# Optimization experiments

Measured on AMD Instinct MI355X. Metric: run time of the kernel, lower is better.

## Reference

```python
import jax, jax.numpy as jnp
import numpy as np

EPS = 1e-4
RES_BAL = 0.3
ATTN_BAL = 0.3
CLIP = 256.0
HEADS = 4
CPH = 64  # channels per head


def _normalize(x, dims):
    # torch normalize: norm = eps + norm * sqrt(norm.numel()/x.numel())
    n = jnp.sqrt(jnp.sum(jnp.square(x), axis=dims, keepdims=True))
    alpha = 1.0 / np.sqrt(float(np.prod([x.shape[d] for d in dims])))
    return x / (EPS + alpha * n)


def _mp_weight(w, gain):
    dims = tuple(range(1, w.ndim))
    fan_in = float(np.prod(w.shape[1:]))
    return _normalize(w, dims) * (gain / np.sqrt(fan_in))


def _conv2d(x, w):
    pad = w.shape[-1] // 2
    return jax.lax.conv_general_dilated(
        x, w, (1, 1), [(pad, pad), (pad, pad)],
        dimension_numbers=('NCHW', 'OIHW', 'NCHW'))


def _mp_silu(x):
    return jax.nn.silu(x) / 0.596


def _mp_sum(a, b, t):
    return ((1.0 - t) * a + t * b) / np.sqrt((1.0 - t) ** 2 + t ** 2)


def setup_inputs() -> dict:
    key = jax.random.key(0)
    ks = jax.random.split(key, 9)
    N, Cin, Cout, Cemb, H, W = 16, 192, 256, 768, 32, 32
    return {
        'x': jax.random.normal(ks[0], (N, Cin, H, W), jnp.float32),
        'emb': jax.random.normal(ks[1], (N, Cemb), jnp.float32),
        'w_skip': jax.random.normal(ks[2], (Cout, Cin, 1, 1), jnp.float32),
        'w_res0': jax.random.normal(ks[3], (Cout, Cout, 3, 3), jnp.float32),
        'w_res1': jax.random.normal(ks[4], (Cout, Cout, 3, 3), jnp.float32),
        'w_emb': jax.random.normal(ks[5], (Cout, Cemb), jnp.float32),
        'emb_gain': jnp.float32(0.5),
        'w_qkv': jax.random.normal(ks[6], (Cout * 3, Cout, 1, 1), jnp.float32),
        'w_proj': jax.random.normal(ks[7], (Cout, Cout, 1, 1), jnp.float32),
    }


def reference(x, emb, w_skip, w_res0, w_res1, w_emb, emb_gain, w_qkv, w_proj):
    N, _, H, W = x.shape
    S = H * W
    # enc flavor: skip conv then pixel-norm over channels
    x = _conv2d(x, _mp_weight(w_skip, 1.0))
    x = _normalize(x, (1,))
    # residual branch
    y = _conv2d(_mp_silu(x), _mp_weight(w_res0, 1.0))
    c = emb @ _mp_weight(w_emb, emb_gain).T + 1.0  # [N, Cout]
    y = y * c[:, :, None, None]
    y = _conv2d(_mp_silu(y), _mp_weight(w_res1, 1.0))
    x = _mp_sum(x, y, RES_BAL)
    # cosine-normalized attention
    qkv = _conv2d(x, _mp_weight(w_qkv, 1.0))              # [N, 3*Cout, H, W]
    qkv = qkv.reshape(N, HEADS, CPH, 3, S)
    qkv = _normalize(qkv, (2,))
    q, k, v = qkv[..., 0, :], qkv[..., 1, :], qkv[..., 2, :]  # [N,h,c,S]
    att = jax.nn.softmax(
        jnp.einsum('nhcq,nhck->nhqk', q, k) / np.sqrt(CPH), axis=3)
    y = jnp.einsum('nhqk,nhck->nhcq', att, v).reshape(x.shape)
    y = _conv2d(y, _mp_weight(w_proj, 1.0))
    x = _mp_sum(x, y, ATTN_BAL)
    return jnp.clip(x, -CLIP, CLIP)
```

## Files before the change

kernel.cpp:

```cpp
#include <hip/hip_runtime.h>
#include <math.h>

#define SDIM 1024
#define COUT 256

#define EPSV     1e-4f
#define SILU_INV 1.6778523489932886f
#define MPA      0.9191450300180579f
#define MPB      0.3939192985791677f
#define LOG2E    1.4426950408889634f

typedef short s16x8 __attribute__((ext_vector_type(8)));
typedef float f32x4 __attribute__((ext_vector_type(4)));
typedef unsigned short ushort_t;

#if __has_builtin(__builtin_amdgcn_exp2f)
#define EXP2F __builtin_amdgcn_exp2f
#else
#define EXP2F exp2f
#endif

__device__ inline ushort_t f2bs(float f) {
    unsigned u = __float_as_uint(f);
    u += 0x7fffu + ((u >> 16) & 1u);
    return (ushort_t)(u >> 16);
}
__device__ inline float silu_mp(float v) { return v * SILU_INV / (1.f + __expf(-v)); }

union F8 { s16x8 v; uint4 q; };
__device__ inline s16x8 ld16(const ushort_t* p) {
    F8 r; r.q = *(const uint4*)p; return r.v;
}

typedef const __attribute__((address_space(1))) unsigned int* gas_ptr;
typedef __attribute__((address_space(3))) unsigned int* las_ptr;
__device__ inline void gld16(const void* g, void* l) {
    __builtin_amdgcn_global_load_lds((gas_ptr)g, (las_ptr)l, 16, 0, 0);
}

__global__ void zfill(uint4* z) { z[threadIdx.x] = make_uint4(0u, 0u, 0u, 0u); }

__global__ __launch_bounds__(256) void wnorm(const float* __restrict__ w,
                                             float* __restrict__ wn,
                                             int fanin,
                                             const float* __restrict__ gain_ptr)
{
    int o = blockIdx.x;
    const float* row = w + (size_t)o * fanin;
    float ss = 0.f;
    for (int i = threadIdx.x; i < fanin; i += 256) { float v = row[i]; ss += v * v; }
    for (int off = 32; off >= 1; off >>= 1) ss += __shfl_down(ss, off);
    __shared__ float red[4];
    int lane = threadIdx.x & 63, wv = threadIdx.x >> 6;
    if (lane == 0) red[wv] = ss;
    __syncthreads();
    float tot = red[0] + red[1] + red[2] + red[3];
    float gain = gain_ptr ? *gain_ptr : 1.0f;
    float scale = gain / (EPSV * sqrtf((float)fanin) + sqrtf(tot));
    for (int i = threadIdx.x; i < fanin; i += 256)
        wn[(size_t)o * fanin + i] = row[i] * scale;
}

template<bool REORDER, bool QPERM>
__global__ __launch_bounds__(256) void wnorm_bf16(const float* __restrict__ w,
                                                  ushort_t* __restrict__ wn,
                                                  int fanin)
{
    int o = blockIdx.x;
    const float* row = w + (size_t)o * fanin;
    float ss = 0.f;
    for (int i = threadIdx.x; i < fanin; i += 256) { float v = row[i]; ss += v * v; }
    for (int off = 32; off >= 1; off >>= 1) ss += __shfl_down(ss, off);
    __shared__ float red[4];
    int lane = threadIdx.x & 63, wv = threadIdx.x >> 6;
    if (lane == 0) red[wv] = ss;
    __syncthreads();
    float tot = red[0] + red[1] + red[2] + red[3];
    float scale = 1.0f / (EPSV * sqrtf((float)fanin) + sqrtf(tot));
    int orow = o;
    if (QPERM) { int h = o / 192, rem = o % 192; orow = (rem % 3) * 256 + h * 64 + rem / 3; }
    for (int i = threadIdx.x; i < fanin; i += 256) {
        int kd = i;
        if (REORDER) { int ci = i / 9; int r9 = i - ci * 9; kd = r9 * 256 + ci; }
        wn[(size_t)orow * fanin + kd] = f2bs(row[i] * scale);
    }
}

__global__ __launch_bounds__(256) void emb_mm(const float* __restrict__ emb,
                                              const float* __restrict__ wemb,
                                              float* __restrict__ cvec)
{
    int n = blockIdx.x;
    int co = threadIdx.x;
    const float* e  = emb  + (size_t)n * 768;
    const float* wr = wemb + (size_t)co * 768;
    float s = 0.f;
    for (int i = 0; i < 768; i++) s = fmaf(e[i], wr[i], s);
    cvec[n * COUT + co] = s + 1.0f;
}

__global__ __launch_bounds__(256) void prep_xT(const float* __restrict__ x,
                                               ushort_t* __restrict__ xT)
{
    const int n = blockIdx.z, ci0 = blockIdx.y * 64, s0 = blockIdx.x * 64;
    const int tid = threadIdx.x;
    __shared__ float T[64 * 65];
#pragma unroll
    for (int i = 0; i < 16; i++) {
        int ch = tid + i * 256; int row = ch >> 6, cc = ch & 63;
        T[row * 65 + cc] = x[((size_t)n * 192 + ci0 + row) * SDIM + s0 + cc];
    }
    __syncthreads();
#pragma unroll
    for (int i = 0; i < 2; i++) {
        int ch = tid + i * 256; int srow = ch >> 3, c8 = ch & 7;
        ushort_t tmp[8];
#pragma unroll
        for (int j = 0; j < 8; j++) tmp[j] = f2bs(T[(c8 * 8 + j) * 65 + srow]);
        *(uint4*)(xT + ((size_t)n * SDIM + s0 + srow) * 192 + ci0 + c8 * 8) = *(uint4*)tmp;
    }
}

__global__ __launch_bounds__(256, 2) void skip_fused(const ushort_t* __restrict__ Wp,
                                                     const ushort_t* __restrict__ xT,
                                                     float* __restrict__ xn,
                                                     ushort_t* __restrict__ sxT)
{
    const int n = blockIdx.z, s0 = blockIdx.x * 32;
    const int tid = threadIdx.x, w = tid >> 6, lane = tid & 63;
    const int tx = lane & 15, quad = lane >> 4;

    __shared__ ushort_t As[256 * 72];
    __shared__ ushort_t Bs[32 * 72];
    __shared__ float csum[4][32];

    f32x4 acc[4][2];
#pragma unroll
    for (int a = 0; a < 4; a++)
#pragma unroll
        for (int b = 0; b < 2; b++) acc[a][b] = (f32x4){0.f, 0.f, 0.f, 0.f};

    for (int k0 = 0; k0 < 192; k0 += 64) {
        __syncthreads();
#pragma unroll
        for (int i = 0; i < 8; i++) {
            int ch = tid + i * 256; int row = ch >> 3, c8 = ch & 7;
            *(uint4*)&As[row * 72 + c8 * 8] = *(const uint4*)(Wp + (size_t)row * 192 + k0 + c8 * 8);
        }
        {
            int row = tid >> 3, c8 = tid & 7;
            *(uint4*)&Bs[row * 72 + c8 * 8] =
                *(const uint4*)(xT + ((size_t)n * SDIM + s0 + row) * 192 + k0 + c8 * 8);
        }
        __syncthreads();
#pragma unroll
        for (int kc = 0; kc < 2; kc++) {
            s16x8 af[4], bf_[2];
#pragma unroll
            for (int mt = 0; mt < 4; mt++) af[mt] = ld16(&As[(w * 64 + mt * 16 + tx) * 72 + kc * 32 + quad * 8]);
#pragma unroll
            for (int nt = 0; nt < 2; nt++) bf_[nt] = ld16(&Bs[(nt * 16 + tx) * 72 + kc * 32 + quad * 8]);
#pragma unroll
            for (int mt = 0; mt < 4; mt++)
#pragma unroll
                for (int nt = 0; nt < 2; nt++)
                    acc[mt][nt] = __builtin_amdgcn_mfma_f32_16x16x32_bf16(af[mt], bf_[nt], acc[mt][nt], 0, 0, 0);
        }
    }

#pragma unroll
    for (int nt = 0; nt < 2; nt++) {
        float s2 = 0.f;
#pragma unroll
        for (int mt = 0; mt < 4; mt++)
#pragma unroll
            for (int r = 0; r < 4; r++) s2 = fmaf(acc[mt][nt][r], acc[mt][nt][r], s2);
        s2 += __shfl_xor(s2, 16); s2 += __shfl_xor(s2, 32);
        if (quad == 0) csum[w][nt * 16 + tx] = s2;
    }
    __syncthreads();
    float f[2];
#pragma unroll
    for (int nt = 0; nt < 2; nt++) {
        int col = nt * 16 + tx;
        float tot = csum[0][col] + csum[1][col] + csum[2][col] + csum[3][col];
        f[nt] = 1.f / (EPSV + sqrtf(tot) * 0.0625f);
    }
    ushort_t* Ls = As;
    float* xb = xn + (size_t)n * COUT * SDIM;
#pragma unroll
    for (int mt = 0; mt < 4; mt++)
#pragma unroll
        for (int r = 0; r < 4; r++) {
            int co = w * 64 + mt * 16 + quad * 4 + r;
#pragma unroll
            for (int nt = 0; nt < 2; nt++) {
                int sp = s0 + nt * 16 + tx;
                float v = acc[mt][nt][r] * f[nt];
                xb[(size_t)co * SDIM + sp] = v;
                Ls[(nt * 16 + tx) * 264 + co] = f2bs(silu_mp(v));
            }
        }
    __syncthreads();
#pragma unroll
    for (int i = 0; i < 4; i++) {
        int ch = tid + i * 256; int row = ch >> 5, c32 = ch & 31;
        *(uint4*)(sxT + ((size_t)n * SDIM + s0 + row) * 256 + c32 * 8) = *(uint4*)&Ls[row * 264 + c32 * 8];
    }
}

template<int KDIM, bool GATHER3, int MODE>
__global__ __launch_bounds__(256, 2) void gemm_glds(const ushort_t* __restrict__ Wp,
                                                    const ushort_t* __restrict__ Bsrc,
                                                    const ushort_t* __restrict__ zbuf,
                                                    float* RX, float* Outf,
                                                    ushort_t* OutT, ushort_t* Vout,
                                                    const float* __restrict__ cvec)
{
    const int n = blockIdx.z, co0 = blockIdx.y * 128, s0 = blockIdx.x * 64;
    const int tid = threadIdx.x, w = tid >> 6, lane = tid & 63;
    const int tx = lane & 15, quad = lane >> 4;
    const int wm = w >> 1, ws = w & 1;
    const int l8 = lane & 7, ld = lane >> 3;
    const int swz = (l8 ^ ld) * 8;

    __shared__ ushort_t SH[2 * 12288];

    const ushort_t* bn = Bsrc + (size_t)n * SDIM * 256;

    auto stageA = [&](int p, int k0) {
        ushort_t* Ab = SH + p * 12288;
#pragma unroll
        for (int j = 0; j < 4; j++) {
            int row0 = w * 32 + j * 8;
            gld16(Wp + (size_t)(co0 + row0 + ld) * KDIM + k0 + swz, Ab + row0 * 64);
        }
    };
    auto stageB = [&](int p, int k0) {
        ushort_t* Bb = SH + p * 12288 + 8192;
        int ci0 = k0, dy = 0, dx = 0;
        if (GATHER3) { int seg = k0 >> 8; ci0 = k0 & 255; int s3 = seg / 3; dy = s3 - 1; dx = seg - s3 * 3 - 1; }
#pragma unroll
        for (int j = 0; j < 2; j++) {
            int row0 = w * 16 + j * 8;
            const ushort_t* g;
            if (GATHER3) {
                int pix = s0 + row0 + ld;
                int h = (pix >> 5) + dy, wx = (pix & 31) + dx;
                bool valid = ((unsigned)h < 32u) && ((unsigned)wx < 32u);
                g = valid ? (bn + (size_t)((h << 5) + wx) * 256 + ci0 + swz) : zbuf;
            } else {
                g = bn + (size_t)(s0 + row0 + ld) * 256 + k0 + swz;
            }
            gld16(g, Bb + row0 * 64);
        }
    };

    f32x4 acc[4][2];
#pragma unroll
    for (int a = 0; a < 4; a++)
#pragma unroll
        for (int b = 0; b < 2; b++) acc[a][b] = (f32x4){0.f, 0.f, 0.f, 0.f};

    constexpr int NK = KDIM / 64;
    stageA(0, 0); stageB(0, 0);
    __syncthreads();

    for (int kt = 0; kt < NK; kt++) {
        int p = kt & 1;
        if (kt + 1 < NK) { stageA(p ^ 1, (kt + 1) * 64); stageB(p ^ 1, (kt + 1) * 64); }
        const ushort_t* Ab = SH + p * 12288;
        const ushort_t* Bb = Ab + 8192;
#pragma unroll
        for (int kc = 0; kc < 2; kc++) {
            int koff = ((kc * 4 + quad) ^ (tx & 7)) * 8;
            s16x8 af[4], bfv[2];
#pragma unroll
            for (int mt = 0; mt < 4; mt++) af[mt]  = ld16(&Ab[(wm * 64 + mt * 16 + tx) * 64 + koff]);
#pragma unroll
            for (int nt = 0; nt < 2; nt++) bfv[nt] = ld16(&Bb[(ws * 32 + nt * 16 + tx) * 64 + koff]);
#pragma unroll
            for (int mt = 0; mt < 4; mt++)
#pragma unroll
                for (int nt = 0; nt < 2; nt++)
                    acc[mt][nt] = __builtin_amdgcn_mfma_f32_16x16x32_bf16(af[mt], bfv[nt], acc[mt][nt], 0, 0, 0);
        }
        __syncthreads();
    }

    if (MODE == 4) {
        float scl[2];
#pragma unroll
        for (int nt = 0; nt < 2; nt++) {
            float s2 = 0.f;
#pragma unroll
            for (int mt = 0; mt < 4; mt++)
#pragma unroll
                for (int r = 0; r < 4; r++) s2 = fmaf(acc[mt][nt][r], acc[mt][nt][r], s2);
            s2 += __shfl_xor(s2, 16); s2 += __shfl_xor(s2, 32);
            float fac = (co0 < 256) ? (0.125f * LOG2E) : 1.0f;
            scl[nt] = fac / (EPSV + sqrtf(s2) * 0.125f);
        }
#pragma unroll
        for (int mt = 0; mt < 4; mt++)
#pragma unroll
            for (int nt = 0; nt < 2; nt++)
#pragma unroll
                for (int r = 0; r < 4; r++) acc[mt][nt][r] *= scl[nt];

        if (co0 < 512) {
            ushort_t* Ls = SH;
#pragma unroll
            for (int mt = 0; mt < 4; mt++)
#pragma unroll
                for (int nt = 0; nt < 2; nt++)
#pragma unroll
                    for (int r = 0; r < 4; r++)
                        Ls[(ws * 32 + nt * 16 + tx) * 136 + wm * 64 + mt * 16 + quad * 4 + r] = f2bs(acc[mt][nt][r]);
            __syncthreads();
#pragma unroll
            for (int i = 0; i < 4; i++) {
                int ch = tid + i * 256; int row = ch >> 4, c16 = ch & 15;
                *(uint4*)(OutT + ((size_t)n * SDIM + s0 + row) * 512 + co0 + c16 * 8) = *(uint4*)&Ls[row * 136 + c16 * 8];
            }
        } else {
            ushort_t* Ls = SH;
#pragma unroll
            for (int mt = 0; mt < 4; mt++)
#pragma unroll
                for (int nt = 0; nt < 2; nt++)
#pragma unroll
                    for (int r = 0; r < 4; r++)
                        Ls[(wm * 64 + mt * 16 + quad * 4 + r) * 72 + ws * 32 + nt * 16 + tx] = f2bs(acc[mt][nt][r]);
            __syncthreads();
#pragma unroll
            for (int i = 0; i < 4; i++) {
                int ch = tid + i * 256; int row = ch >> 3, c8 = ch & 7;
                *(uint4*)(Vout + ((size_t)n * 256 + (co0 - 512) + row) * SDIM + s0 + c8 * 8) = *(uint4*)&Ls[row * 72 + c8 * 8];
            }
        }
    }
    if (MODE == 1) {
        float cm[4][4];
#pragma unroll
        for (int mt = 0; mt < 4; mt++)
#pragma unroll
            for (int r = 0; r < 4; r++)
                cm[mt][r] = cvec[n * COUT + co0 + wm * 64 + mt * 16 + quad * 4 + r];
        ushort_t* Ls = SH;
#pragma unroll
        for (int mt = 0; mt < 4; mt++)
#pragma unroll
            for (int nt = 0; nt < 2; nt++)
#pragma unroll
                for (int r = 0; r < 4; r++) {
                    float v = silu_mp(acc[mt][nt][r] * cm[mt][r]);
                    Ls[(ws * 32 + nt * 16 + tx) * 136 + wm * 64 + mt * 16 + quad * 4 + r] = f2bs(v);
                }
        __syncthreads();
#pragma unroll
        for (int i = 0; i < 4; i++) {
            int ch = tid + i * 256; int row = ch >> 4, c16 = ch & 15;
            *(uint4*)(OutT + ((size_t)n * SDIM + s0 + row) * 256 + co0 + c16 * 8) = *(uint4*)&Ls[row * 136 + c16 * 8];
        }
    }
    if (MODE == 2) {
        ushort_t* Ls = SH;
#pragma unroll
        for (int mt = 0; mt < 4; mt++)
#pragma unroll
            for (int r = 0; r < 4; r++) {
                int col = wm * 64 + mt * 16 + quad * 4 + r;
                float* xp = RX + ((size_t)n * COUT + co0 + col) * SDIM + s0 + ws * 32;
#pragma unroll
                for (int nt = 0; nt < 2; nt++) {
                    float v = MPA * xp[nt * 16 + tx] + MPB * acc[mt][nt][r];
                    xp[nt * 16 + tx] = v;
                    Ls[(ws * 32 + nt * 16 + tx) * 136 + col] = f2bs(v);
                }
            }
        __syncthreads();
#pragma unroll
        for (int i = 0; i < 4; i++) {
            int ch = tid + i * 256; int row = ch >> 4, c16 = ch & 15;
            *(uint4*)(OutT + ((size_t)n * SDIM + s0 + row) * 256 + co0 + c16 * 8) = *(uint4*)&Ls[row * 136 + c16 * 8];
        }
    }
    if (MODE == 3) {
#pragma unroll
        for (int mt = 0; mt < 4; mt++)
#pragma unroll
            for (int r = 0; r < 4; r++) {
                int co = co0 + wm * 64 + mt * 16 + quad * 4 + r;
                const float* xp = RX + ((size_t)n * COUT + co) * SDIM + s0 + ws * 32;
                float* op = Outf + ((size_t)n * COUT + co) * SDIM + s0 + ws * 32;
#pragma unroll
                for (int nt = 0; nt < 2; nt++) {
                    float v = MPA * xp[nt * 16 + tx] + MPB * acc[mt][nt][r];
                    op[nt * 16 + tx] = fminf(fmaxf(v, -256.f), 256.f);
                }
            }
    }
}

__global__ __launch_bounds__(256, 2) void attn_mfma(const ushort_t* __restrict__ qkT,
                                                    const ushort_t* __restrict__ vbuf,
                                                    ushort_t* __restrict__ aT)
{
    const int n = blockIdx.z, head = blockIdx.y, q0 = blockIdx.x * 128;
    const int tid = threadIdx.x, w = tid >> 6, lane = tid & 63;
    const int tx = lane & 15, quad = lane >> 4;

    __shared__ ushort_t Pl[4][32 * 72];

    const size_t nb = (size_t)n * SDIM;
    const int qw = q0 + w * 32;

    s16x8 qf[2][2];
#pragma unroll
    for (int mt = 0; mt < 2; mt++)
#pragma unroll
        for (int kc = 0; kc < 2; kc++)
            qf[mt][kc] = ld16(qkT + (nb + qw + mt * 16 + tx) * 512 + head * 64 + kc * 32 + quad * 8);

    f32x4 acco[2][4];
    float lpart[2][4];
#pragma unroll
    for (int mt = 0; mt < 2; mt++)
#pragma unroll
        for (int nt = 0; nt < 4; nt++) acco[mt][nt] = (f32x4){0.f, 0.f, 0.f, 0.f};
#pragma unroll
    for (int mt = 0; mt < 2; mt++)
#pragma unroll
        for (int r = 0; r < 4; r++) lpart[mt][r] = 0.f;

    const ushort_t* kbase = qkT + nb * 512 + 256 + head * 64;
    const ushort_t* vbase = vbuf + ((size_t)n * 256 + head * 64) * SDIM;

    for (int kt = 0; kt < 16; kt++) {
        int k0 = kt * 64;
        s16x8 kf[4][2];
#pragma unroll
        for (int nt = 0; nt < 4; nt++)
#pragma unroll
            for (int kc = 0; kc < 2; kc++)
                kf[nt][kc] = ld16(kbase + (size_t)(k0 + nt * 16 + tx) * 512 + kc * 32 + quad * 8);

        f32x4 accs[2][4];
#pragma unroll
        for (int mt = 0; mt < 2; mt++)
#pragma unroll
            for (int nt = 0; nt < 4; nt++) accs[mt][nt] = (f32x4){0.f, 0.f, 0.f, 0.f};
#pragma unroll
        for (int kc = 0; kc < 2; kc++)
#pragma unroll
            for (int nt = 0; nt < 4; nt++)
#pragma unroll
                for (int mt = 0; mt < 2; mt++)
                    accs[mt][nt] = __builtin_amdgcn_mfma_f32_16x16x32_bf16(
                        qf[mt][kc], kf[nt][kc], accs[mt][nt], 0, 0, 0);

#pragma unroll
        for (int mt = 0; mt < 2; mt++)
#pragma unroll
            for (int nt = 0; nt < 4; nt++)
#pragma unroll
                for (int r = 0; r < 4; r++) {
                    float p = EXP2F(accs[mt][nt][r]);
                    lpart[mt][r] += p;
                    Pl[w][(mt * 16 + quad * 4 + r) * 72 + nt * 16 + tx] = f2bs(p);
                }
        asm volatile("s_waitcnt lgkmcnt(0)" ::: "memory");

        s16x8 vf[4][2], pf[2][2];
#pragma unroll
        for (int nt = 0; nt < 4; nt++)
#pragma unroll
            for (int kc = 0; kc < 2; kc++)
                vf[nt][kc] = ld16(vbase + (size_t)(nt * 16 + tx) * SDIM + k0 + kc * 32 + quad * 8);
#pragma unroll
        for (int mt = 0; mt < 2; mt++)
#pragma unroll
            for (int kc = 0; kc < 2; kc++)
                pf[mt][kc] = ld16(&Pl[w][(mt * 16 + tx) * 72 + kc * 32 + quad * 8]);
#pragma unroll
        for (int kc = 0; kc < 2; kc++)
#pragma unroll
            for (int nt = 0; nt < 4; nt++)
#pragma unroll
                for (int mt = 0; mt < 2; mt++)
                    acco[mt][nt] = __builtin_amdgcn_mfma_f32_16x16x32_bf16(
                        pf[mt][kc], vf[nt][kc], acco[mt][nt], 0, 0, 0);
    }

    float inv[2][4];
#pragma unroll
    for (int mt = 0; mt < 2; mt++)
#pragma unroll
        for (int r = 0; r < 4; r++) {
            float l = lpart[mt][r];
            l += __shfl_xor(l, 1); l += __shfl_xor(l, 2);
            l += __shfl_xor(l, 4); l += __shfl_xor(l, 8);
            inv[mt][r] = 1.0f / l;
        }

#pragma unroll
    for (int mt = 0; mt < 2; mt++)
#pragma unroll
        for (int nt = 0; nt < 4; nt++)
#pragma unroll
            for (int r = 0; r < 4; r++)
                Pl[w][(mt * 16 + quad * 4 + r) * 72 + nt * 16 + tx] = f2bs(acco[mt][nt][r] * inv[mt][r]);
    asm volatile("s_waitcnt lgkmcnt(0)" ::: "memory");
    ushort_t* dst = aT + (nb + qw) * 256 + head * 64;
#pragma unroll
    for (int i = 0; i < 4; i++) {
        int ch = lane + i * 64; int row = ch >> 3, c8 = ch & 7;
        *(uint4*)(dst + (size_t)row * 256 + c8 * 8) = *(uint4*)&Pl[w][row * 72 + c8 * 8];
    }
}

extern "C" void kernel_launch(void* const* d_in, const int* in_sizes, int n_in,
                              void* d_out, int out_size, void* d_ws, size_t ws_size,
                              hipStream_t stream)
{
    const float* x      = (const float*)d_in[0];
    const float* emb    = (const float*)d_in[1];
    const float* w_skip = (const float*)d_in[2];
    const float* w_res0 = (const float*)d_in[3];
    const float* w_res1 = (const float*)d_in[4];
    const float* w_emb  = (const float*)d_in[5];
    const float* e_gain = (const float*)d_in[6];
    const float* w_qkv  = (const float*)d_in[7];
    const float* w_proj = (const float*)d_in[8];
    float* out = (float*)d_out;

    char* p = (char*)d_ws;
    auto alloc = [&](size_t bytes) { void* r = (void*)p; p += (bytes + 255) & ~(size_t)255; return r; };
    ushort_t* wskip_bf = (ushort_t*)alloc(256 * 192 * 2);
    ushort_t* wres0_bf = (ushort_t*)alloc(256 * 2304 * 2);
    ushort_t* wres1_bf = (ushort_t*)alloc(256 * 2304 * 2);
    ushort_t* wqkv_bf  = (ushort_t*)alloc(768 * 256 * 2);
    ushort_t* wproj_bf = (ushort_t*)alloc(256 * 256 * 2);
    float*    wemb_n   = (float*)alloc(256 * 768 * 4);
    float*    cvec     = (float*)alloc(16 * 256 * 4);
    ushort_t* zbuf     = (ushort_t*)alloc(1024);
    ushort_t* xT   = (ushort_t*)alloc((size_t)16 * 1024 * 192 * 2);
    ushort_t* sxT  = (ushort_t*)alloc((size_t)16 * 1024 * 256 * 2);
    ushort_t* ysT  = (ushort_t*)alloc((size_t)16 * 1024 * 256 * 2);
    ushort_t* x2T  = (ushort_t*)alloc((size_t)16 * 1024 * 256 * 2);
    ushort_t* aT   = (ushort_t*)alloc((size_t)16 * 1024 * 256 * 2);
    float*    xn   = (float*)alloc((size_t)16 * 256 * 1024 * 4);
    ushort_t* qkT  = (ushort_t*)alloc((size_t)16 * 1024 * 512 * 2);
    ushort_t* vbuf = (ushort_t*)alloc((size_t)16 * 256 * 1024 * 2);

    zfill<<<1, 64, 0, stream>>>((uint4*)zbuf);
    wnorm_bf16<false, false><<<256, 256, 0, stream>>>(w_skip, wskip_bf, 192);
    wnorm_bf16<true,  false><<<256, 256, 0, stream>>>(w_res0, wres0_bf, 2304);
    wnorm_bf16<true,  false><<<256, 256, 0, stream>>>(w_res1, wres1_bf, 2304);
    wnorm_bf16<false, true ><<<768, 256, 0, stream>>>(w_qkv,  wqkv_bf,  256);
    wnorm_bf16<false, false><<<256, 256, 0, stream>>>(w_proj, wproj_bf, 256);
    wnorm<<<256, 256, 0, stream>>>(w_emb, wemb_n, 768, e_gain);

    emb_mm<<<16, 256, 0, stream>>>(emb, wemb_n, cvec);
    prep_xT<<<dim3(16, 3, 16), 256, 0, stream>>>(x, xT);

    skip_fused<<<dim3(32, 1, 16), 256, 0, stream>>>(wskip_bf, xT, xn, sxT);
    gemm_glds<2304, true, 1><<<dim3(16, 2, 16), 256, 0, stream>>>(wres0_bf, sxT, zbuf, nullptr, nullptr, ysT, nullptr, cvec);
    gemm_glds<2304, true, 2><<<dim3(16, 2, 16), 256, 0, stream>>>(wres1_bf, ysT, zbuf, xn, nullptr, x2T, nullptr, nullptr);
    gemm_glds<256, false, 4><<<dim3(16, 6, 16), 256, 0, stream>>>(wqkv_bf, x2T, zbuf, nullptr, nullptr, qkT, vbuf, nullptr);
    attn_mfma<<<dim3(8, 4, 16), 256, 0, stream>>>(qkT, vbuf, aT);
    gemm_glds<256, false, 3><<<dim3(16, 2, 16), 256, 0, stream>>>(wproj_bf, aT, zbuf, xn, out, nullptr, nullptr, nullptr);
}
```

Baseline: 301.2 us.

## Stage K/V in swizzled LDS for attention and merge prep kernels

The attention kernel now gives each wave 64 query rows instead of 32, so each block covers 256 queries. K and V tiles are double-buffered in LDS through global_load_lds with an XOR swizzle, and the four waves share them instead of each wave loading K/V from global memory on its own. The P scratch buffer uses the same swizzle to avoid bank conflicts. Separately, all weight-normalisation kernels, the x transpose and the zero fill are merged into one launch, and the emb weight normalisation is folded into emb_mm. The attention grid halves to 256 blocks at occupancy 1 with more registers per thread, which may leave some CUs idle.

```diff
diff --git a/kernel.cpp b/kernel.cpp
--- a/kernel.cpp
+++ b/kernel.cpp
@@ -38,87 +38,82 @@
     __builtin_amdgcn_global_load_lds((gas_ptr)g, (las_ptr)l, 16, 0, 0);
 }
 
-__global__ void zfill(uint4* z) { z[threadIdx.x] = make_uint4(0u, 0u, 0u, 0u); }
-
-__global__ __launch_bounds__(256) void wnorm(const float* __restrict__ w,
-                                             float* __restrict__ wn,
-                                             int fanin,
-                                             const float* __restrict__ gain_ptr)
+__global__ __launch_bounds__(256) void prep_all(
+    const float* __restrict__ w_skip, const float* __restrict__ w_res0,
+    const float* __restrict__ w_res1, const float* __restrict__ w_qkv,
+    const float* __restrict__ w_proj, const float* __restrict__ x,
+    ushort_t* wskip_bf, ushort_t* wres0_bf, ushort_t* wres1_bf,
+    ushort_t* wqkv_bf, ushort_t* wproj_bf, ushort_t* xT, uint4* zbuf)
 {
-    int o = blockIdx.x;
-    const float* row = w + (size_t)o * fanin;
+    __shared__ float T[64 * 65];
+    const int b = blockIdx.x, tid = threadIdx.x;
+
+    if (b >= 2560) {
+        if (tid < 64) zbuf[tid] = make_uint4(0u, 0u, 0u, 0u);
+        return;
+    }
+    if (b >= 1792) {
+        int b2 = b - 1792;
+        int n = b2 / 48, rem = b2 % 48;
+        int ci0 = (rem / 16) * 64, s0 = (rem & 15) * 64;
+#pragma unroll
+        for (int i = 0; i < 16; i++) {
+            int ch = tid + i * 256; int row = ch >> 6, cc = ch & 63;
+            T[row * 65 + cc] = x[((size_t)n * 192 + ci0 + row) * SDIM + s0 + cc];
+        }
+        __syncthreads();
+#pragma unroll
+        for (int i = 0; i < 2; i++) {
+            int ch = tid + i * 256; int srow = ch >> 3, c8 = ch & 7;
+            ushort_t tmp[8];
+#pragma unroll
+            for (int j = 0; j < 8; j++) tmp[j] = f2bs(T[(c8 * 8 + j) * 65 + srow]);
+            *(uint4*)(xT + ((size_t)n * SDIM + s0 + srow) * 192 + ci0 + c8 * 8) = *(uint4*)tmp;
+        }
+        return;
+    }
+    const float* src; ushort_t* dst; int fanin, mode, o;
+    if      (b < 256)  { src = w_skip; dst = wskip_bf; fanin = 192;  mode = 0; o = b; }
+    else if (b < 512)  { src = w_res0; dst = wres0_bf; fanin = 2304; mode = 1; o = b - 256; }
+    else if (b < 768)  { src = w_res1; dst = wres1_bf; fanin = 2304; mode = 1; o = b - 512; }
+    else if (b < 1536) { src = w_qkv;  dst = wqkv_bf;  fanin = 256;  mode = 2; o = b - 768; }
+    else               { src = w_proj; dst = wproj_bf; fanin = 256;  mode = 0; o = b - 1536; }
+
+    const float* row = src + (size_t)o * fanin;
     float ss = 0.f;
-    for (int i = threadIdx.x; i < fanin; i += 256) { float v = row[i]; ss += v * v; }
+    for (int i = tid; i < fanin; i += 256) { float v = row[i]; ss += v * v; }
     for (int off = 32; off >= 1; off >>= 1) ss += __shfl_down(ss, off);
-    __shared__ float red[4];
-    int lane = threadIdx.x & 63, wv = threadIdx.x >> 6;
-    if (lane == 0) red[wv] = ss;
+    int lane = tid & 63, wv = tid >> 6;
+    if (lane == 0) T[wv] = ss;
     __syncthreads();
-    float tot = red[0] + red[1] + red[2] + red[3];
-    float gain = gain_ptr ? *gain_ptr : 1.0f;
-    float scale = gain / (EPSV * sqrtf((float)fanin) + sqrtf(tot));
-    for (int i = threadIdx.x; i < fanin; i += 256)
-        wn[(size_t)o * fanin + i] = row[i] * scale;
-}
-
-template<bool REORDER, bool QPERM>
-__global__ __launch_bounds__(256) void wnorm_bf16(const float* __restrict__ w,
-                                                  ushort_t* __restrict__ wn,
-                                                  int fanin)
-{
-    int o = blockIdx.x;
-    const float* row = w + (size_t)o * fanin;
-    float ss = 0.f;
-    for (int i = threadIdx.x; i < fanin; i += 256) { float v = row[i]; ss += v * v; }
-    for (int off = 32; off >= 1; off >>= 1) ss += __shfl_down(ss, off);
-    __shared__ float red[4];
-    int lane = threadIdx.x & 63, wv = threadIdx.x >> 6;
-    if (lane == 0) red[wv] = ss;
-    __syncthreads();
-    float tot = red[0] + red[1] + red[2] + red[3];
+    float tot = T[0] + T[1] + T[2] + T[3];
     float scale = 1.0f / (EPSV * sqrtf((float)fanin) + sqrtf(tot));
     int orow = o;
-    if (QPERM) { int h = o / 192, rem = o % 192; orow = (rem % 3) * 256 + h * 64 + rem / 3; }
-    for (int i = threadIdx.x; i < fanin; i += 256) {
+    if (mode == 2) { int h = o / 192, rem = o % 192; orow = (rem % 3) * 256 + h * 64 + rem / 3; }
+    for (int i = tid; i < fanin; i += 256) {
         int kd = i;
-        if (REORDER) { int ci = i / 9; int r9 = i - ci * 9; kd = r9 * 256 + ci; }
-        wn[(size_t)orow * fanin + kd] = f2bs(row[i] * scale);
+        if (mode == 1) { int ci = i / 9; int r9 = i - ci * 9; kd = r9 * 256 + ci; }
+        dst[(size_t)orow * fanin + kd] = f2bs(row[i] * scale);
     }
 }
 
 __global__ __launch_bounds__(256) void emb_mm(const float* __restrict__ emb,
-                                              const float* __restrict__ wemb,
+                                              const float* __restrict__ w_emb,
+                                              const float* __restrict__ gain_ptr,
                                               float* __restrict__ cvec)
 {
     int n = blockIdx.x;
     int co = threadIdx.x;
-    const float* e  = emb  + (size_t)n * 768;
-    const float* wr = wemb + (size_t)co * 768;
-    float s = 0.f;
-    for (int i = 0; i < 768; i++) s = fmaf(e[i], wr[i], s);
-    cvec[n * COUT + co] = s + 1.0f;
-}
-
-__global__ __launch_bounds__(256) void prep_xT(const float* __restrict__ x,
-                                               ushort_t* __restrict__ xT)
-{
-    const int n = blockIdx.z, ci0 = blockIdx.y * 64, s0 = blockIdx.x * 64;
-    const int tid = threadIdx.x;
-    __shared__ float T[64 * 65];
-#pragma unroll
-    for (int i = 0; i < 16; i++) {
-        int ch = tid + i * 256; int row = ch >> 6, cc = ch & 63;
-        T[row * 65 + cc] = x[((size_t)n * 192 + ci0 + row) * SDIM + s0 + cc];
-    }
-    __syncthreads();
-#pragma unroll
-    for (int i = 0; i < 2; i++) {
-        int ch = tid + i * 256; int srow = ch >> 3, c8 = ch & 7;
-        ushort_t tmp[8];
-#pragma unroll
-        for (int j = 0; j < 8; j++) tmp[j] = f2bs(T[(c8 * 8 + j) * 65 + srow]);
-        *(uint4*)(xT + ((size_t)n * SDIM + s0 + srow) * 192 + ci0 + c8 * 8) = *(uint4*)tmp;
-    }
+    const float* e  = emb   + (size_t)n * 768;
+    const float* wr = w_emb + (size_t)co * 768;
+    float ss = 0.f, dot = 0.f;
+    for (int i = 0; i < 768; i++) {
+        float wv = wr[i];
+        ss  = fmaf(wv, wv, ss);
+        dot = fmaf(e[i], wv, dot);
+    }
+    float scale = gain_ptr[0] / (EPSV * sqrtf(768.0f) + sqrtf(ss));
+    cvec[n * COUT + co] = dot * scale + 1.0f;
 }
 
 __global__ __launch_bounds__(256, 2) void skip_fused(const ushort_t* __restrict__ Wp,
@@ -403,99 +398,115 @@
     }
 }
 
-__global__ __launch_bounds__(256, 2) void attn_mfma(const ushort_t* __restrict__ qkT,
+__global__ __launch_bounds__(256, 1) void attn_mfma(const ushort_t* __restrict__ qkT,
                                                     const ushort_t* __restrict__ vbuf,
                                                     ushort_t* __restrict__ aT)
 {
-    const int n = blockIdx.z, head = blockIdx.y, q0 = blockIdx.x * 128;
+    const int n = blockIdx.z, head = blockIdx.y, q0 = blockIdx.x * 256;
     const int tid = threadIdx.x, w = tid >> 6, lane = tid & 63;
     const int tx = lane & 15, quad = lane >> 4;
-
-    __shared__ ushort_t Pl[4][32 * 72];
+    const int l8 = lane & 7, ld = lane >> 3;
+    const int swz = (l8 ^ ld) * 8;
+
+    __shared__ ushort_t Kst[2][4096];
+    __shared__ ushort_t Vst[2][4096];
+    __shared__ ushort_t Pl[4][4096];
 
     const size_t nb = (size_t)n * SDIM;
-    const int qw = q0 + w * 32;
-
-    s16x8 qf[2][2];
-#pragma unroll
-    for (int mt = 0; mt < 2; mt++)
+    const int qw = q0 + w * 64;
+    const ushort_t* kg = qkT + nb * 512 + 256 + head * 64;
+    const ushort_t* vg = vbuf + ((size_t)n * 256 + head * 64) * SDIM;
+
+    auto stage = [&](int p, int k0) {
+#pragma unroll
+        for (int j = 0; j < 2; j++) {
+            int row0 = w * 16 + j * 8;
+            gld16(kg + (size_t)(k0 + row0 + ld) * 512 + swz, &Kst[p][row0 * 64]);
+            gld16(vg + (size_t)(row0 + ld) * SDIM + k0 + swz, &Vst[p][row0 * 64]);
+        }
+    };
+
+    s16x8 qf[4][2];
+#pragma unroll
+    for (int mt = 0; mt < 4; mt++)
 #pragma unroll
         for (int kc = 0; kc < 2; kc++)
             qf[mt][kc] = ld16(qkT + (nb + qw + mt * 16 + tx) * 512 + head * 64 + kc * 32 + quad * 8);
 
-    f32x4 acco[2][4];
-    float lpart[2][4];
-#pragma unroll
-    for (int mt = 0; mt < 2; mt++)
+    f32x4 acco[4][4];
+    float lpart[4][4];
+#pragma unroll
+    for (int mt = 0; mt < 4; mt++)
 #pragma unroll
         for (int nt = 0; nt < 4; nt++) acco[mt][nt] = (f32x4){0.f, 0.f, 0.f, 0.f};
 #pragma unroll
-    for (int mt = 0; mt < 2; mt++)
+    for (int mt = 0; mt < 4; mt++)
 #pragma unroll
         for (int r = 0; r < 4; r++) lpart[mt][r] = 0.f;
 
-    const ushort_t* kbase = qkT + nb * 512 + 256 + head * 64;
-    const ushort_t* vbase = vbuf + ((size_t)n * 256 + head * 64) * SDIM;
+    stage(0, 0);
+    __syncthreads();
 
     for (int kt = 0; kt < 16; kt++) {
-        int k0 = kt * 64;
-        s16x8 kf[4][2];
-#pragma unroll
-        for (int nt = 0; nt < 4; nt++)
-#pragma unroll
-            for (int kc = 0; kc < 2; kc++)
-                kf[nt][kc] = ld16(kbase + (size_t)(k0 + nt * 16 + tx) * 512 + kc * 32 + quad * 8);
-
-        f32x4 accs[2][4];
-#pragma unroll
-        for (int mt = 0; mt < 2; mt++)
+        int p = kt & 1;
+        if (kt < 15) stage(p ^ 1, (kt + 1) * 64);
+
+        f32x4 accs[4][4];
+#pragma unroll
+        for (int mt = 0; mt < 4; mt++)
 #pragma unroll
             for (int nt = 0; nt < 4; nt++) accs[mt][nt] = (f32x4){0.f, 0.f, 0.f, 0.f};
 #pragma unroll
-        for (int kc = 0; kc < 2; kc++)
-#pragma unroll
-            for (int nt = 0; nt < 4; nt++)
-#pragma unroll
-                for (int mt = 0; mt < 2; mt++)
+        for (int kc = 0; kc < 2; kc++) {
+            int koff = ((kc * 4 + quad) ^ (tx & 7)) * 8;
+#pragma unroll
+            for (int nt = 0; nt < 4; nt++) {
+                s16x8 kf = ld16(&Kst[p][(nt * 16 + tx) * 64 + koff]);
+#pragma unroll
+                for (int mt = 0; mt < 4; mt++)
                     accs[mt][nt] = __builtin_amdgcn_mfma_f32_16x16x32_bf16(
-                        qf[mt][kc], kf[nt][kc], accs[mt][nt], 0, 0, 0);
-
-#pragma unroll
-        for (int mt = 0; mt < 2; mt++)
-#pragma unroll
-            for (int nt = 0; nt < 4; nt++)
-#pragma unroll
-                for (int r = 0; r < 4; r++) {
-                    float p = EXP2F(accs[mt][nt][r]);
-                    lpart[mt][r] += p;
-                    Pl[w][(mt * 16 + quad * 4 + r) * 72 + nt * 16 + tx] = f2bs(p);
+                        qf[mt][kc], kf, accs[mt][nt], 0, 0, 0);
+            }
+        }
+
+#pragma unroll
+        for (int mt = 0; mt < 4; mt++)
+#pragma unroll
+            for (int r = 0; r < 4; r++) {
+                int row = mt * 16 + quad * 4 + r;
+                int rx = row & 7;
+#pragma unroll
+                for (int nt = 0; nt < 4; nt++) {
+                    float pv = EXP2F(accs[mt][nt][r]);
+                    lpart[mt][r] += pv;
+                    int slot = (nt * 2 + (tx >> 3)) ^ rx;
+                    Pl[w][row * 64 + slot * 8 + (tx & 7)] = f2bs(pv);
                 }
+            }
         asm volatile("s_waitcnt lgkmcnt(0)" ::: "memory");
 
-        s16x8 vf[4][2], pf[2][2];
-#pragma unroll
-        for (int nt = 0; nt < 4; nt++)
-#pragma unroll
-            for (int kc = 0; kc < 2; kc++)
-                vf[nt][kc] = ld16(vbase + (size_t)(nt * 16 + tx) * SDIM + k0 + kc * 32 + quad * 8);
-#pragma unroll
-        for (int mt = 0; mt < 2; mt++)
-#pragma unroll
-            for (int kc = 0; kc < 2; kc++)
-                pf[mt][kc] = ld16(&Pl[w][(mt * 16 + tx) * 72 + kc * 32 + quad * 8]);
-#pragma unroll
-        for (int kc = 0; kc < 2; kc++)
-#pragma unroll
-            for (int nt = 0; nt < 4; nt++)
-#pragma unroll
-                for (int mt = 0; mt < 2; mt++)
+#pragma unroll
+        for (int kc = 0; kc < 2; kc++) {
+            int koff = ((kc * 4 + quad) ^ (tx & 7)) * 8;
+            s16x8 pf[4];
+#pragma unroll
+            for (int mt = 0; mt < 4; mt++)
+                pf[mt] = ld16(&Pl[w][(mt * 16 + tx) * 64 + koff]);
+#pragma unroll
+            for (int nt = 0; nt < 4; nt++) {
+                s16x8 vf = ld16(&Vst[p][(nt * 16 + tx) * 64 + koff]);
+#pragma unroll
+                for (int mt = 0; mt < 4; mt++)
                     acco[mt][nt] = __builtin_amdgcn_mfma_f32_16x16x32_bf16(
-                        pf[mt][kc], vf[nt][kc], acco[mt][nt], 0, 0, 0);
-    }
-
-    float inv[2][4];
-#pragma unroll
-    for (int mt = 0; mt < 2; mt++)
+                        pf[mt], vf, acco[mt][nt], 0, 0, 0);
+            }
+        }
+        __syncthreads();
+    }
+
+    float inv[4][4];
+#pragma unroll
+    for (int mt = 0; mt < 4; mt++)
 #pragma unroll
         for (int r = 0; r < 4; r++) {
             float l = lpart[mt][r];
@@ -505,18 +516,23 @@
         }
 
 #pragma unroll
-    for (int mt = 0; mt < 2; mt++)
-#pragma unroll
-        for (int nt = 0; nt < 4; nt++)
-#pragma unroll
-            for (int r = 0; r < 4; r++)
-                Pl[w][(mt * 16 + quad * 4 + r) * 72 + nt * 16 + tx] = f2bs(acco[mt][nt][r] * inv[mt][r]);
+    for (int mt = 0; mt < 4; mt++)
+#pragma unroll
+        for (int r = 0; r < 4; r++) {
+            int row = mt * 16 + quad * 4 + r;
+            int rx = row & 7;
+#pragma unroll
+            for (int nt = 0; nt < 4; nt++) {
+                int slot = (nt * 2 + (tx >> 3)) ^ rx;
+                Pl[w][row * 64 + slot * 8 + (tx & 7)] = f2bs(acco[mt][nt][r] * inv[mt][r]);
+            }
+        }
     asm volatile("s_waitcnt lgkmcnt(0)" ::: "memory");
     ushort_t* dst = aT + (nb + qw) * 256 + head * 64;
 #pragma unroll
-    for (int i = 0; i < 4; i++) {
+    for (int i = 0; i < 8; i++) {
         int ch = lane + i * 64; int row = ch >> 3, c8 = ch & 7;
-        *(uint4*)(dst + (size_t)row * 256 + c8 * 8) = *(uint4*)&Pl[w][row * 72 + c8 * 8];
+        *(uint4*)(dst + (size_t)row * 256 + c8 * 8) = *(uint4*)&Pl[w][row * 64 + (c8 ^ (row & 7)) * 8];
     }
 }
 
@@ -542,7 +558,6 @@
     ushort_t* wres1_bf = (ushort_t*)alloc(256 * 2304 * 2);
     ushort_t* wqkv_bf  = (ushort_t*)alloc(768 * 256 * 2);
     ushort_t* wproj_bf = (ushort_t*)alloc(256 * 256 * 2);
-    float*    wemb_n   = (float*)alloc(256 * 768 * 4);
     float*    cvec     = (float*)alloc(16 * 256 * 4);
     ushort_t* zbuf     = (ushort_t*)alloc(1024);
     ushort_t* xT   = (ushort_t*)alloc((size_t)16 * 1024 * 192 * 2);
@@ -554,21 +569,15 @@
     ushort_t* qkT  = (ushort_t*)alloc((size_t)16 * 1024 * 512 * 2);
     ushort_t* vbuf = (ushort_t*)alloc((size_t)16 * 256 * 1024 * 2);
 
-    zfill<<<1, 64, 0, stream>>>((uint4*)zbuf);
-    wnorm_bf16<false, false><<<256, 256, 0, stream>>>(w_skip, wskip_bf, 192);
-    wnorm_bf16<true,  false><<<256, 256, 0, stream>>>(w_res0, wres0_bf, 2304);
-    wnorm_bf16<true,  false><<<256, 256, 0, stream>>>(w_res1, wres1_bf, 2304);
-    wnorm_bf16<false, true ><<<768, 256, 0, stream>>>(w_qkv,  wqkv_bf,  256);
-    wnorm_bf16<false, false><<<256, 256, 0, stream>>>(w_proj, wproj_bf, 256);
-    wnorm<<<256, 256, 0, stream>>>(w_emb, wemb_n, 768, e_gain);
-
-    emb_mm<<<16, 256, 0, stream>>>(emb, wemb_n, cvec);
-    prep_xT<<<dim3(16, 3, 16), 256, 0, stream>>>(x, xT);
+    prep_all<<<2561, 256, 0, stream>>>(w_skip, w_res0, w_res1, w_qkv, w_proj, x,
+                                       wskip_bf, wres0_bf, wres1_bf, wqkv_bf, wproj_bf,
+                                       xT, (uint4*)zbuf);
+    emb_mm<<<16, 256, 0, stream>>>(emb, w_emb, e_gain, cvec);
 
     skip_fused<<<dim3(32, 1, 16), 256, 0, stream>>>(wskip_bf, xT, xn, sxT);
     gemm_glds<2304, true, 1><<<dim3(16, 2, 16), 256, 0, stream>>>(wres0_bf, sxT, zbuf, nullptr, nullptr, ysT, nullptr, cvec);
     gemm_glds<2304, true, 2><<<dim3(16, 2, 16), 256, 0, stream>>>(wres1_bf, ysT, zbuf, xn, nullptr, x2T, nullptr, nullptr);
     gemm_glds<256, false, 4><<<dim3(16, 6, 16), 256, 0, stream>>>(wqkv_bf, x2T, zbuf, nullptr, nullptr, qkT, vbuf, nullptr);
-    attn_mfma<<<dim3(8, 4, 16), 256, 0, stream>>>(qkT, vbuf, aT);
+    attn_mfma<<<dim3(4, 4, 16), 256, 0, stream>>>(qkT, vbuf, aT);
     gemm_glds<256, false, 3><<<dim3(16, 2, 16), 256, 0, stream>>>(wproj_bf, aT, zbuf, xn, out, nullptr, nullptr, nullptr);
 }
```

Result: faster. 261.5 us (-13.2%).
